# Performance work log

Hardware: AMD Instinct MI355X
Metric: run time of the kernel (lower is better)

## Reference

```python
import jax, jax.numpy as jnp
import numpy as np

B = 512      # batch size
D = 128      # per-input feature dim (hard-coded as 2*128 in the torch module)
H = 512      # hidden_dim


def setup_inputs() -> dict:
    key = jax.random.key(0)
    kx, ky, kw1, kw2 = jax.random.split(key, 4)
    x = jax.random.normal(kx, (B, D), dtype=jnp.float32)
    y = jax.random.normal(ky, (B, D), dtype=jnp.float32)
    # Linear layer params (torch Linear default-ish init scale)
    W1 = jax.random.normal(kw1, (2 * D, H), dtype=jnp.float32) * (1.0 / np.sqrt(2 * D))
    b1 = jnp.zeros((H,), dtype=jnp.float32)
    W2 = jax.random.normal(kw2, (H, 1), dtype=jnp.float32) * (1.0 / np.sqrt(H))
    b2 = jnp.zeros((1,), dtype=jnp.float32)
    return {"x": x, "y": y, "W1": W1, "b1": b1, "W2": W2, "b2": b2}


def reference(x, y, W1, b1, W2, b2):
    # Faithful to torch: pairs[i, j] = concat(x[j], y[i])
    b = x.shape[0]
    x_t = jnp.broadcast_to(x[None, :, :], (b, b, x.shape[1]))   # tile x along dim 0
    y_t = jnp.broadcast_to(y[:, None, :], (b, b, y.shape[1]))   # tile y along dim 1
    pairs = jnp.concatenate([x_t, y_t], axis=2).reshape(b * b, 2 * x.shape[1])  # [B*B, 2D]
    h = jax.nn.relu(pairs @ W1 + b1)          # [B*B, H]
    scores = h @ W2 + b2                       # [B*B, 1]
    # reshape to (B, B) then transpose, as in torch.t(...)
    # result[a, b] = mlp(concat(x[a], y[b]))
    return scores.reshape(b, b).T
```

## Files before the change

kernel.cpp:

```cpp
#include <hip/hip_runtime.h>
#include <hip/hip_bf16.h>


#define B 512
#define D 128
#define H 512
#define CH 64

__global__ void k1_uv(const float* __restrict__ x, const float* __restrict__ y,
                      const float* __restrict__ W1, const float* __restrict__ b1,
                      float* __restrict__ U, float* __restrict__ V) {
    const int m  = blockIdx.y;
    const int a0 = blockIdx.x * 4;
    const float* __restrict__ src = (m == 0) ? x : y;
    float* __restrict__ dst       = (m == 0) ? U : V;
    const float* __restrict__ Wm  = W1 + (size_t)m * D * H;

    __shared__ float xs[4][D];
    const int t = threadIdx.x;
    for (int i = t; i < 4 * D; i += 256)
        xs[i >> 7][i & (D - 1)] = src[(size_t)(a0 + (i >> 7)) * D + (i & (D - 1))];
    __syncthreads();

    const int h = t;
    float acc[4][2];
#pragma unroll
    for (int r = 0; r < 4; ++r) {
        acc[r][0] = (m == 0) ? b1[h] : 0.0f;
        acc[r][1] = (m == 0) ? b1[h + 256] : 0.0f;
    }
#pragma unroll 4
    for (int d = 0; d < D; ++d) {
        const float w0 = Wm[(size_t)d * H + h];
        const float w1 = Wm[(size_t)d * H + h + 256];
#pragma unroll
        for (int r = 0; r < 4; ++r) {
            const float xv = xs[r][d];
            acc[r][0] = fmaf(xv, w0, acc[r][0]);
            acc[r][1] = fmaf(xv, w1, acc[r][1]);
        }
    }
#pragma unroll
    for (int r = 0; r < 4; ++r) {
        dst[(size_t)(a0 + r) * H + h]       = acc[r][0];
        dst[(size_t)(a0 + r) * H + h + 256] = acc[r][1];
    }
}

__global__ void k2_pair(const float* __restrict__ U, const float* __restrict__ V,
                        const float* __restrict__ W2, float* __restrict__ P,
                        int hcount) {
    __shared__ float Us[CH][64];
    __shared__ float Vs[CH][64];
    __shared__ float w2s[CH];

    const int a0 = blockIdx.x * 64;
    const int b0 = blockIdx.y * 64;
    const int h0 = blockIdx.z * hcount;
    const int tid = threadIdx.x;
    const int ta = tid & 15;
    const int tb = tid >> 4;

    float acc[4][4] = {};

    const int r = tid >> 2;
    const int q = tid & 3;

    for (int c = 0; c < hcount; c += CH) {
        const float* __restrict__ Urow = U + (size_t)(a0 + r) * H + h0 + c;
        const float* __restrict__ Vrow = V + (size_t)(b0 + r) * H + h0 + c;
#pragma unroll
        for (int p = 0; p < 4; ++p) {
            const int hh = 4 * q + 16 * p;
            const float4 u4 = *(const float4*)(Urow + hh);
            const float4 v4 = *(const float4*)(Vrow + hh);
            Us[hh + 0][r] = u4.x; Us[hh + 1][r] = u4.y;
            Us[hh + 2][r] = u4.z; Us[hh + 3][r] = u4.w;
            Vs[hh + 0][r] = v4.x; Vs[hh + 1][r] = v4.y;
            Vs[hh + 2][r] = v4.z; Vs[hh + 3][r] = v4.w;
        }
        if (tid < CH) w2s[tid] = W2[h0 + c + tid];
        __syncthreads();

        for (int h = 0; h < CH; ++h) {
            const float4 ua = *(const float4*)&Us[h][4 * ta];
            const float4 vb = *(const float4*)&Vs[h][4 * tb];
            const float w = w2s[h];
            const float u[4] = {ua.x, ua.y, ua.z, ua.w};
            const float v[4] = {vb.x, vb.y, vb.z, vb.w};
#pragma unroll
            for (int i = 0; i < 4; ++i)
#pragma unroll
                for (int j = 0; j < 4; ++j)
                    acc[i][j] = fmaf(fmaxf(u[i] + v[j], 0.0f), w, acc[i][j]);
        }
        __syncthreads();
    }

    float* __restrict__ out = P + (size_t)blockIdx.z * (B * B);
#pragma unroll
    for (int i = 0; i < 4; ++i) {
        float4 o;
        o.x = acc[i][0]; o.y = acc[i][1]; o.z = acc[i][2]; o.w = acc[i][3];
        *(float4*)(out + (size_t)(a0 + 4 * ta + i) * B + b0 + 4 * tb) = o;
    }
}

__global__ void k3_reduce(const float* __restrict__ P, const float* __restrict__ b2,
                          float* __restrict__ out, int S) {
    const int i = blockIdx.x * 256 + threadIdx.x;
    float s = b2[0];
    for (int k = 0; k < S; ++k) s += P[(size_t)k * (B * B) + i];
    out[i] = s;
}

extern "C" void kernel_launch(void* const* d_in, const int* in_sizes, int n_in,
                              void* d_out, int out_size, void* d_ws, size_t ws_size,
                              hipStream_t stream) {
    const float* x  = (const float*)d_in[0];
    const float* y  = (const float*)d_in[1];
    const float* W1 = (const float*)d_in[2];
    const float* b1 = (const float*)d_in[3];
    const float* W2 = (const float*)d_in[4];
    const float* b2 = (const float*)d_in[5];
    float* out = (float*)d_out;

    float* U = (float*)d_ws;
    float* V = U + (size_t)B * H;
    float* P = V + (size_t)B * H;

    const size_t base = 2ull * B * H * sizeof(float);
    int S = 1;
    if (ws_size >= base + 8ull * B * B * sizeof(float)) S = 8;
    else if (ws_size >= base + 4ull * B * B * sizeof(float)) S = 4;
    else if (ws_size >= base + 2ull * B * B * sizeof(float)) S = 2;

    k1_uv<<<dim3(B / 4, 2), 256, 0, stream>>>(x, y, W1, b1, U, V);
    k2_pair<<<dim3(8, 8, S), 256, 0, stream>>>(U, V, W2, P, H / S);
    k3_reduce<<<dim3((B * B) / 256), 256, 0, stream>>>(P, b2, out, S);
}
```

Measured before the change: 33.01 us.

## Rewrite ReLU as half-sum plus half-abs and precompute linear terms

Uses relu(s) = 0.5*(s + |s|) so the inner pair loop computes only |u+v|*w2. The linear parts (u·w2 and v·w2) are reduced once per row in the first kernel and added back in the reduce kernel. The change also splits the first kernel across a z dimension for more blocks, pads the shared tiles to reduce bank conflicts, reads W2 directly instead of staging it in shared memory, and vectorises the final reduce with float4. The math is exact but rounding changes slightly, and the first kernel gains extra shuffle-reduction work.

```diff
diff --git a/kernel.cpp b/kernel.cpp
--- a/kernel.cpp
+++ b/kernel.cpp
@@ -6,53 +6,62 @@
 #define D 128
 #define H 512
 #define CH 64
+#define LDP 68
 
-__global__ void k1_uv(const float* __restrict__ x, const float* __restrict__ y,
-                      const float* __restrict__ W1, const float* __restrict__ b1,
-                      float* __restrict__ U, float* __restrict__ V) {
+__global__ __launch_bounds__(256) void k1_uv(
+        const float* __restrict__ x, const float* __restrict__ y,
+        const float* __restrict__ W1, const float* __restrict__ b1,
+        const float* __restrict__ W2,
+        float* __restrict__ U, float* __restrict__ V, float* __restrict__ PQ) {
     const int m  = blockIdx.y;
+    const int z  = blockIdx.z;
     const int a0 = blockIdx.x * 4;
     const float* __restrict__ src = (m == 0) ? x : y;
     float* __restrict__ dst       = (m == 0) ? U : V;
     const float* __restrict__ Wm  = W1 + (size_t)m * D * H;
 
     __shared__ float xs[4][D];
+    __shared__ float red[4][4];
     const int t = threadIdx.x;
     for (int i = t; i < 4 * D; i += 256)
         xs[i >> 7][i & (D - 1)] = src[(size_t)(a0 + (i >> 7)) * D + (i & (D - 1))];
     __syncthreads();
 
-    const int h = t;
-    float acc[4][2];
-#pragma unroll
-    for (int r = 0; r < 4; ++r) {
-        acc[r][0] = (m == 0) ? b1[h] : 0.0f;
-        acc[r][1] = (m == 0) ? b1[h + 256] : 0.0f;
-    }
+    const int h = z * 256 + t;
+    float bias = (m == 0) ? b1[h] : 0.0f;
+    float acc[4] = {bias, bias, bias, bias};
 #pragma unroll 4
     for (int d = 0; d < D; ++d) {
-        const float w0 = Wm[(size_t)d * H + h];
-        const float w1 = Wm[(size_t)d * H + h + 256];
+        const float w = Wm[(size_t)d * H + h];
 #pragma unroll
-        for (int r = 0; r < 4; ++r) {
-            const float xv = xs[r][d];
-            acc[r][0] = fmaf(xv, w0, acc[r][0]);
-            acc[r][1] = fmaf(xv, w1, acc[r][1]);
-        }
+        for (int r = 0; r < 4; ++r) acc[r] = fmaf(xs[r][d], w, acc[r]);
     }
 #pragma unroll
-    for (int r = 0; r < 4; ++r) {
-        dst[(size_t)(a0 + r) * H + h]       = acc[r][0];
-        dst[(size_t)(a0 + r) * H + h + 256] = acc[r][1];
+    for (int r = 0; r < 4; ++r) dst[(size_t)(a0 + r) * H + h] = acc[r];
+
+    const float wp = 0.5f * W2[h];
+    float v[4];
+#pragma unroll
+    for (int r = 0; r < 4; ++r) v[r] = acc[r] * wp;
+#pragma unroll
+    for (int r = 0; r < 4; ++r)
+        for (int o = 32; o > 0; o >>= 1) v[r] += __shfl_down(v[r], o);
+    const int wave = t >> 6;
+    if ((t & 63) == 0)
+#pragma unroll
+        for (int r = 0; r < 4; ++r) red[wave][r] = v[r];
+    __syncthreads();
+    if (t < 4) {
+        const float s = red[0][t] + red[1][t] + red[2][t] + red[3][t];
+        PQ[(size_t)(m * 2 + z) * B + a0 + t] = s;
     }
 }
 
-__global__ void k2_pair(const float* __restrict__ U, const float* __restrict__ V,
-                        const float* __restrict__ W2, float* __restrict__ P,
-                        int hcount) {
-    __shared__ float Us[CH][64];
-    __shared__ float Vs[CH][64];
-    __shared__ float w2s[CH];
+__global__ __launch_bounds__(256) void k2_pair(
+        const float* __restrict__ U, const float* __restrict__ V,
+        const float* __restrict__ W2, float* __restrict__ P, int hcount) {
+    __shared__ float Us[CH][LDP];
+    __shared__ float Vs[CH][LDP];
 
     const int a0 = blockIdx.x * 64;
     const int b0 = blockIdx.y * 64;
@@ -60,11 +69,10 @@
     const int tid = threadIdx.x;
     const int ta = tid & 15;
     const int tb = tid >> 4;
+    const int r = tid >> 2;
+    const int q = tid & 3;
 
     float acc[4][4] = {};
-
-    const int r = tid >> 2;
-    const int q = tid & 3;
 
     for (int c = 0; c < hcount; c += CH) {
         const float* __restrict__ Urow = U + (size_t)(a0 + r) * H + h0 + c;
@@ -79,20 +87,20 @@
             Vs[hh + 0][r] = v4.x; Vs[hh + 1][r] = v4.y;
             Vs[hh + 2][r] = v4.z; Vs[hh + 3][r] = v4.w;
         }
-        if (tid < CH) w2s[tid] = W2[h0 + c + tid];
         __syncthreads();
 
-        for (int h = 0; h < CH; ++h) {
-            const float4 ua = *(const float4*)&Us[h][4 * ta];
-            const float4 vb = *(const float4*)&Vs[h][4 * tb];
-            const float w = w2s[h];
+#pragma unroll 4
+        for (int hh = 0; hh < CH; ++hh) {
+            const float w = W2[h0 + c + hh];
+            const float4 ua = *(const float4*)&Us[hh][4 * ta];
+            const float4 vb = *(const float4*)&Vs[hh][4 * tb];
             const float u[4] = {ua.x, ua.y, ua.z, ua.w};
             const float v[4] = {vb.x, vb.y, vb.z, vb.w};
 #pragma unroll
             for (int i = 0; i < 4; ++i)
 #pragma unroll
                 for (int j = 0; j < 4; ++j)
-                    acc[i][j] = fmaf(fmaxf(u[i] + v[j], 0.0f), w, acc[i][j]);
+                    acc[i][j] = fmaf(__builtin_fabsf(u[i] + v[j]), w, acc[i][j]);
         }
         __syncthreads();
     }
@@ -106,12 +114,28 @@
     }
 }
 
-__global__ void k3_reduce(const float* __restrict__ P, const float* __restrict__ b2,
-                          float* __restrict__ out, int S) {
-    const int i = blockIdx.x * 256 + threadIdx.x;
-    float s = b2[0];
-    for (int k = 0; k < S; ++k) s += P[(size_t)k * (B * B) + i];
-    out[i] = s;
+__global__ __launch_bounds__(256) void k3_reduce(
+        const float* __restrict__ Pp, const float* __restrict__ PQ,
+        const float* __restrict__ b2, float* __restrict__ out, int S) {
+    const int gi = blockIdx.x * 256 + threadIdx.x;
+    const int i = gi * 4;
+    const int a = i >> 9;
+    const int b = i & (B - 1);
+
+    float4 s = {0.f, 0.f, 0.f, 0.f};
+    for (int z = 0; z < S; ++z) {
+        const float4 p = *(const float4*)(Pp + (size_t)z * (B * B) + i);
+        s.x += p.x; s.y += p.y; s.z += p.z; s.w += p.w;
+    }
+    const float pa = PQ[a] + PQ[B + a] + b2[0];
+    const float4 qb0 = *(const float4*)(PQ + 2 * B + b);
+    const float4 qb1 = *(const float4*)(PQ + 3 * B + b);
+    float4 o;
+    o.x = pa + qb0.x + qb1.x + 0.5f * s.x;
+    o.y = pa + qb0.y + qb1.y + 0.5f * s.y;
+    o.z = pa + qb0.z + qb1.z + 0.5f * s.z;
+    o.w = pa + qb0.w + qb1.w + 0.5f * s.w;
+    *(float4*)(out + i) = o;
 }
 
 extern "C" void kernel_launch(void* const* d_in, const int* in_sizes, int n_in,
@@ -125,17 +149,18 @@
     const float* b2 = (const float*)d_in[5];
     float* out = (float*)d_out;
 
-    float* U = (float*)d_ws;
-    float* V = U + (size_t)B * H;
-    float* P = V + (size_t)B * H;
+    float* U  = (float*)d_ws;
+    float* V  = U + (size_t)B * H;
+    float* PQ = V + (size_t)B * H;
+    float* Pp = PQ + 4 * B;
 
-    const size_t base = 2ull * B * H * sizeof(float);
+    const size_t base = (2ull * B * H + 4 * B) * sizeof(float);
     int S = 1;
     if (ws_size >= base + 8ull * B * B * sizeof(float)) S = 8;
     else if (ws_size >= base + 4ull * B * B * sizeof(float)) S = 4;
     else if (ws_size >= base + 2ull * B * B * sizeof(float)) S = 2;
 
-    k1_uv<<<dim3(B / 4, 2), 256, 0, stream>>>(x, y, W1, b1, U, V);
-    k2_pair<<<dim3(8, 8, S), 256, 0, stream>>>(U, V, W2, P, H / S);
-    k3_reduce<<<dim3((B * B) / 256), 256, 0, stream>>>(P, b2, out, S);
+    k1_uv<<<dim3(B / 4, 2, 2), 256, 0, stream>>>(x, y, W1, b1, W2, U, V, PQ);
+    k2_pair<<<dim3(8, 8, S), 256, 0, stream>>>(U, V, W2, Pp, H / S);
+    k3_reduce<<<dim3((B * B) / (256 * 4)), 256, 0, stream>>>(Pp, PQ, b2, out, S);
 }
```

Result: faster. 31.69 us (-4.0%).
